# Optimization experiments

Hardware: AMD Instinct MI355X
Metric: run time of the kernel (lower is better)

## Reference

```python
import jax, jax.numpy as jnp
import numpy as np

N_QUBITS = 10
N_LAYERS = 4
BATCH = 2048


def setup_inputs() -> dict:
    key = jax.random.key(0)
    k1, k2 = jax.random.split(key)
    x = jax.random.normal(k1, (BATCH, N_QUBITS), dtype=jnp.float32)
    q_params = jax.random.normal(k2, (N_LAYERS * N_QUBITS * 3,), dtype=jnp.float32) * 0.01
    return {"x": x, "q_params": q_params}


def _apply_1q(state, U, wire):
    # state: (B, 2, 2, ..., 2); U: (2, 2) complex. Applies U on `wire`.
    s = jnp.moveaxis(state, wire + 1, -1)
    s = jnp.einsum('...j,ij->...i', s, U)
    return jnp.moveaxis(s, -1, wire + 1)


def _apply_cnot(state, ctrl, tgt):
    # flip target amplitude pair where control bit == 1
    s = jnp.moveaxis(state, (ctrl + 1, tgt + 1), (-2, -1))
    s = jnp.concatenate([s[..., 0:1, :], s[..., 1:2, ::-1]], axis=-2)
    return jnp.moveaxis(s, (-2, -1), (ctrl + 1, tgt + 1))


def _forward(x, q_params):
    B = x.shape[0]
    n, L = N_QUBITS, N_LAYERS
    # --- data-encoding layer: RY(x_i)|0> = [cos(x_i/2), sin(x_i/2)] per qubit ---
    half = 0.5 * x
    amps = jnp.stack([jnp.cos(half), jnp.sin(half)], axis=-1).astype(jnp.complex64)  # (B, n, 2)
    state = amps[:, 0, :]
    for i in range(1, n):  # build product state via successive kron (loop over n_qubits only)
        state = (state[:, :, None] * amps[:, i, None, :]).reshape(B, -1)
    state = state.reshape((B,) + (2,) * n)
    # --- variational gate matrices: per (layer, qubit) fused U = RZ @ RY @ RX ---
    w = q_params.reshape(L, n, 3)
    c, s = jnp.cos(0.5 * w), jnp.sin(0.5 * w)
    cx = c[..., 0].astype(jnp.complex64); sx = s[..., 0].astype(jnp.complex64)
    cy = c[..., 1].astype(jnp.complex64); sy = s[..., 1].astype(jnp.complex64)
    ez = jnp.exp(-0.5j * w[..., 2].astype(jnp.complex64))
    zeros = jnp.zeros_like(ez)
    Urx = jnp.stack([jnp.stack([cx, -1j * sx], -1), jnp.stack([-1j * sx, cx], -1)], -2)  # (L,n,2,2)
    Ury = jnp.stack([jnp.stack([cy, -sy], -1), jnp.stack([sy, cy], -1)], -2)
    Urz = jnp.stack([jnp.stack([ez, zeros], -1), jnp.stack([zeros, jnp.conj(ez)], -1)], -2)
    U = jnp.einsum('lnab,lnbc,lncd->lnad', Urz, Ury, Urx)  # apply order: RX then RY then RZ
    # --- circuit layers ---
    for l in range(L):
        for i in range(n):
            state = _apply_1q(state, U[l, i], i)
        for i in range(n - 1):
            state = _apply_cnot(state, i, i + 1)
    # --- <Z_i> expectation values ---
    p = jnp.abs(state) ** 2  # (B, 2, ..., 2) real probabilities
    evs = []
    for i in range(n):
        axes = tuple(a for a in range(1, n + 1) if a != i + 1)
        pi = jnp.sum(p, axis=axes)  # (B, 2)
        evs.append(pi[:, 0] - pi[:, 1])
    return jnp.stack(evs, axis=-1)  # (B, n_qubits)


def reference(x, q_params):
    return _forward(x, q_params)
```

## Files before the change

### kernel.cpp

```cpp
#include <hip/hip_runtime.h>
#include <math.h>

#define NQ 10
#define NL 4
#define NGATES (NL * NQ)
#define NTHREADS 256
#define BPW 2
#define WAVES 4

typedef float f32x2 __attribute__((ext_vector_type(2)));

#if __has_builtin(__builtin_amdgcn_permlane32_swap)
#define HAVE_PLSWAP 1
#else
#define HAVE_PLSWAP 0
#endif


template<int XM>
__device__ __forceinline__ float exch1(float v, bool selP) {
    if constexpr (XM == 0) return v;
    int x = __float_as_int(v);
    constexpr int low = XM & 31;
    if constexpr (low == 1)      x = __builtin_amdgcn_mov_dpp(x, 0xB1, 0xF, 0xF, true);
    else if constexpr (low == 2) x = __builtin_amdgcn_mov_dpp(x, 0x4E, 0xF, 0xF, true);
    else if constexpr (low == 3) x = __builtin_amdgcn_mov_dpp(x, 0x1B, 0xF, 0xF, true);
    else if constexpr (low != 0) x = __builtin_amdgcn_ds_swizzle(x, (low << 10) | 0x1F);
    if constexpr ((XM & 32) != 0) {
#if HAVE_PLSWAP
        auto r = __builtin_amdgcn_permlane32_swap((unsigned)x, (unsigned)x, false, false);
        x = selP ? (int)r[0] : (int)r[1];
#else
        x = __float_as_int(__shfl_xor(__int_as_float(x), 32, 64));
#endif
    }
    return __int_as_float(x);
}

template<int XM>
__device__ __forceinline__ f32x2 exch2(f32x2 v, bool selP) {
    f32x2 r;
    r.x = exch1<XM>(v.x, selP);
    r.y = exch1<XM>(v.y, selP);
    return r;
}

__device__ __forceinline__ f32x2 cfma4(f32x2 A, f32x2 st, f32x2 B, f32x2 pst) {
    f32x2 t;
    asm("v_pk_mul_f32 %0, %1, %2 op_sel:[0,0] op_sel_hi:[0,1]\n\t"
        "v_pk_fma_f32 %0, %1, %2, %0 op_sel:[1,1,0] op_sel_hi:[1,0,1] neg_lo:[0,1,0]\n\t"
        "v_pk_fma_f32 %0, %3, %4, %0 op_sel:[0,0,0] op_sel_hi:[0,1,1]\n\t"
        "v_pk_fma_f32 %0, %3, %4, %0 op_sel:[1,1,0] op_sel_hi:[1,0,1] neg_lo:[0,1,0]"
        : "=&v"(t)
        : "v"(A), "v"(st), "v"(B), "v"(pst));
    return t;
}

template<int XM, int XR, int SL, int SR>
__device__ __forceinline__ void gate2(f32x2 (&sa)[16], f32x2 (&sb)[16],
                                      const f32x2 (&g4)[4], int lane, bool selP) {
    bool hl = (SL != 0) && ((__popc(lane & SL) & 1) != 0);
    f32x2 A0, B0, A1, B1;
    A0.x = hl ? g4[3].x : g4[0].x;  A0.y = hl ? g4[3].y : g4[0].y;
    B0.x = hl ? g4[2].x : g4[1].x;  B0.y = hl ? g4[2].y : g4[1].y;
    A1.x = hl ? g4[0].x : g4[3].x;  A1.y = hl ? g4[0].y : g4[3].y;
    B1.x = hl ? g4[1].x : g4[2].x;  B1.y = hl ? g4[1].y : g4[2].y;
    f32x2 pa[16], pb[16];
    #pragma unroll
    for (int r = 0; r < 16; ++r) {
        pa[r] = exch2<XM>(sa[r ^ XR], selP);
        pb[r] = exch2<XM>(sb[r ^ XR], selP);
    }
    #pragma unroll
    for (int r = 0; r < 16; ++r) {
        const bool p1 = (__builtin_popcount(r & SR) & 1) != 0;
        f32x2 Ar = p1 ? A1 : A0;
        f32x2 Br = p1 ? B1 : B0;
        sa[r] = cfma4(Ar, sa[r], Br, pa[r]);
        sb[r] = cfma4(Ar, sb[r], Br, pb[r]);
    }
}

__device__ __forceinline__ float wht6(float v, int lane, bool selP) {
    float t;
    t = exch1<1>(v, selP);   v = (lane & 1)  ? (t - v) : (v + t);
    t = exch1<2>(v, selP);   v = (lane & 2)  ? (t - v) : (v + t);
    t = exch1<4>(v, selP);   v = (lane & 4)  ? (t - v) : (v + t);
    t = exch1<8>(v, selP);   v = (lane & 8)  ? (t - v) : (v + t);
    t = exch1<16>(v, selP);  v = (lane & 16) ? (t - v) : (v + t);
    t = exch1<32>(v, selP);  v = (lane & 32) ? (t - v) : (v + t);
    return v;
}

__device__ __forceinline__ void init_state(const float* __restrict__ x, int b,
                                           int lane, f32x2 (&st)[16]) {
    float c[NQ], s[NQ];
    #pragma unroll
    for (int q = 0; q < NQ; ++q) {
        float h = 0.5f * x[b * NQ + q];
        c[q] = __cosf(h);  s[q] = __sinf(h);
    }
    float lf = ((lane & 16) ? s[0] : c[0]) * ((lane & 8) ? s[1] : c[1]) *
               ((lane &  4) ? s[2] : c[2]) * ((lane & 32) ? s[7] : c[7]) *
               ((lane &  2) ? s[8] : c[8]) * ((lane &  1) ? s[9] : c[9]);
    #pragma unroll
    for (int r = 0; r < 16; ++r) {
        st[r].x = lf * ((r & 8) ? s[3] : c[3]) * ((r & 4) ? s[4] : c[4]) *
                       ((r & 2) ? s[5] : c[5]) * ((r & 1) ? s[6] : c[6]);
        st[r].y = 0.0f;
    }
}

__device__ __forceinline__ void epilogue(const f32x2 (&st)[16], int lane,
                                         bool selP, float* __restrict__ o) {
    float p[16];
    #pragma unroll
    for (int r = 0; r < 16; ++r) p[r] = st[r].x * st[r].x + st[r].y * st[r].y;
    float a[8], f8 = 0.0f;
    #pragma unroll
    for (int r = 0; r < 8; ++r) { a[r] = p[r] + p[r + 8]; f8 += p[r] - p[r + 8]; }
    float c4[4], f4 = 0.0f;
    #pragma unroll
    for (int r = 0; r < 4; ++r) { c4[r] = a[r] + a[r + 4]; f4 += a[r] - a[r + 4]; }
    float e2[2], f2 = 0.0f;
    #pragma unroll
    for (int r = 0; r < 2; ++r) { e2[r] = c4[r] + c4[r + 2]; f2 += c4[r] - c4[r + 2]; }
    float P  = e2[0] + e2[1];
    float f1 = e2[0] - e2[1];

    float wP = wht6(P,  lane, selP);
    float w8 = wht6(f8, lane, selP);
    float w4 = wht6(f4, lane, selP);
    float w2 = wht6(f2, lane, selP);
    float w1 = wht6(f1, lane, selP);

    if (lane == 16) { o[0] = wP; o[4] = w4; }
    if (lane ==  8) { o[1] = wP; o[5] = w2; }
    if (lane ==  4) { o[2] = wP; o[6] = w1; }
    if (lane ==  0) { o[3] = w8; }
    if (lane == 32) { o[7] = w8; }
    if (lane == 18) { o[8] = w4; }
    if (lane ==  9) { o[9] = w2; }
}

__global__ __launch_bounds__(NTHREADS, 1) void qlayer_kernel(
    const float* __restrict__ x,
    const float* __restrict__ qp,
    float* __restrict__ out,
    int B)
{
    __shared__ f32x2 su[NGATES][4];

    const int t = threadIdx.x;
    if (t < NGATES) {
        float w0 = qp[t * 3 + 0], w1 = qp[t * 3 + 1], w2 = qp[t * 3 + 2];
        float cx = __cosf(0.5f * w0), sx = __sinf(0.5f * w0);
        float cy = __cosf(0.5f * w1), sy = __sinf(0.5f * w1);
        float er = __cosf(0.5f * w2), ei = -__sinf(0.5f * w2);
        float m00r =  cy * cx, m00i =  sy * sx;
        float m01r = -sy * cx, m01i = -cy * sx;
        float m10r =  sy * cx, m10i = -cy * sx;
        float m11r =  cy * cx, m11i = -sy * sx;
        f32x2 v;
        v.x = er * m00r - ei * m00i;  v.y = er * m00i + ei * m00r;  su[t][0] = v;
        v.x = er * m01r - ei * m01i;  v.y = er * m01i + ei * m01r;  su[t][1] = v;
        v.x = er * m10r + ei * m10i;  v.y = er * m10i - ei * m10r;  su[t][2] = v;
        v.x = er * m11r + ei * m11i;  v.y = er * m11i - ei * m11r;  su[t][3] = v;
    }
    __syncthreads();

    const int lane = t & 63;
    const int wave = t >> 6;
    const int b0 = (blockIdx.x * WAVES + wave) * BPW;
    if (b0 >= B) return;

    bool selP = false;
#if HAVE_PLSWAP
    {
        auto pr = __builtin_amdgcn_permlane32_swap((unsigned)lane, (unsigned)lane, false, false);
        selP = ((int)pr[0] == (lane ^ 32));
    }
#endif

    f32x2 sa[16], sb[16];
    init_state(x, b0, lane, sa);
    init_state(x, (b0 + 1 < B) ? b0 + 1 : b0, lane, sb);

#define PREFETCH(L)                                                   \
    f32x2 cf[NQ][4];                                                  \
    _Pragma("unroll")                                                 \
    for (int q = 0; q < NQ; ++q) {                                    \
        cf[q][0] = su[(L)*NQ + q][0];  cf[q][1] = su[(L)*NQ + q][1];  \
        cf[q][2] = su[(L)*NQ + q][2];  cf[q][3] = su[(L)*NQ + q][3];  \
    }
#define GATE(Q, XM, XR, SLm, SRm) \
    gate2<XM, XR, SLm, SRm>(sa, sb, cf[Q], lane, selP);

    {
        PREFETCH(0)
        GATE(0, 16,0, 16,0)  GATE(1, 8,0, 8,0)    GATE(2, 4,0, 4,0)
        GATE(3, 0,8, 0,8)    GATE(4, 0,4, 0,4)    GATE(5, 0,2, 0,2)
        GATE(6, 0,1, 0,1)    GATE(7, 32,0, 32,0)  GATE(8, 2,0, 2,0)
        GATE(9, 1,0, 1,0)
    }
    {
        PREFETCH(1)
        GATE(0, 24,0, 16,0)  GATE(1, 12,0, 24,0)  GATE(2, 4,8, 28,0)
        GATE(3, 0,12, 28,8)  GATE(4, 0,6, 28,12)  GATE(5, 0,3, 28,14)
        GATE(6, 32,1, 28,15) GATE(7, 34,0, 60,15) GATE(8, 3,0, 62,15)
        GATE(9, 1,0, 63,15)
    }
    {
        PREFETCH(2)
        GATE(0, 20,0, 16,0)  GATE(1, 8,8, 8,0)    GATE(2, 4,4, 20,0)
        GATE(3, 0,10, 8,8)   GATE(4, 0,5, 20,4)   GATE(5, 32,2, 8,10)
        GATE(6, 2,1, 20,5)   GATE(7, 33,0, 40,10) GATE(8, 2,0, 22,5)
        GATE(9, 1,0, 41,10)
    }
    {
        PREFETCH(3)
        GATE(0, 28,8, 16,0)  GATE(1, 12,12, 24,0) GATE(2, 4,14, 12,0)
        GATE(3, 0,15, 4,8)   GATE(4, 32,7, 16,12) GATE(5, 34,3, 24,6)
        GATE(6, 35,1, 12,3)  GATE(7, 35,0, 36,9)  GATE(8, 3,0, 50,12)
        GATE(9, 1,0, 27,6)
    }
#undef GATE
#undef PREFETCH

    epilogue(sa, lane, selP, out + b0 * NQ);
    if (b0 + 1 < B) epilogue(sb, lane, selP, out + (b0 + 1) * NQ);
}

extern "C" void kernel_launch(void* const* d_in, const int* in_sizes, int n_in,
                              void* d_out, int out_size, void* d_ws, size_t ws_size,
                              hipStream_t stream) {
    const float* x  = (const float*)d_in[0];
    const float* qp = (const float*)d_in[1];
    float* out = (float*)d_out;
    const int B = in_sizes[0] / NQ;
    const int bpb = WAVES * BPW;
    const int blocks = (B + bpb - 1) / bpb;
    qlayer_kernel<<<blocks, NTHREADS, 0, stream>>>(x, qp, out, B);
}
```

Before: 80.74 us.

## Remap qubits to lanes for DPP/permlane exchanges, one sample per wave

Qubit-to-lane bits are reassigned so that most cross-lane exchanges use DPP row operations (row_mirror, row_half_mirror, quad perms) or permlane16/32 swaps instead of ds_swizzle. Each wave now simulates one batch sample instead of two, which doubles the grid, halves register state, and allows two blocks per CU via launch bounds. The aim is lower cross-lane exchange latency and more waves in flight to hide it, at the cost of less ILP per wave and a recomputed gate schedule and output lane mapping that must stay correct.

```diff
diff --git a/kernel.cpp b/kernel.cpp
--- a/kernel.cpp
+++ b/kernel.cpp
@@ -5,31 +5,52 @@
 #define NL 4
 #define NGATES (NL * NQ)
 #define NTHREADS 256
-#define BPW 2
-#define WAVES 4
+#define WPB 4
 
 typedef float f32x2 __attribute__((ext_vector_type(2)));
 
 #if __has_builtin(__builtin_amdgcn_permlane32_swap)
-#define HAVE_PLSWAP 1
-#else
-#define HAVE_PLSWAP 0
+#define HAVE_PL32 1
+#else
+#define HAVE_PL32 0
+#endif
+#if __has_builtin(__builtin_amdgcn_permlane16_swap)
+#define HAVE_PL16 1
+#else
+#define HAVE_PL16 0
 #endif
 
 
 template<int XM>
-__device__ __forceinline__ float exch1(float v, bool selP) {
+__device__ __forceinline__ float exch1(float v, bool sp32, bool sp16) {
     if constexpr (XM == 0) return v;
     int x = __float_as_int(v);
     constexpr int low = XM & 31;
-    if constexpr (low == 1)      x = __builtin_amdgcn_mov_dpp(x, 0xB1, 0xF, 0xF, true);
-    else if constexpr (low == 2) x = __builtin_amdgcn_mov_dpp(x, 0x4E, 0xF, 0xF, true);
-    else if constexpr (low == 3) x = __builtin_amdgcn_mov_dpp(x, 0x1B, 0xF, 0xF, true);
-    else if constexpr (low != 0) x = __builtin_amdgcn_ds_swizzle(x, (low << 10) | 0x1F);
+    if constexpr (low == 1)       x = __builtin_amdgcn_mov_dpp(x, 0xB1, 0xF, 0xF, true);
+    else if constexpr (low == 2)  x = __builtin_amdgcn_mov_dpp(x, 0x4E, 0xF, 0xF, true);
+    else if constexpr (low == 3)  x = __builtin_amdgcn_mov_dpp(x, 0x1B, 0xF, 0xF, true);
+    else if constexpr (low == 7)  x = __builtin_amdgcn_mov_dpp(x, 0x141, 0xF, 0xF, true);
+    else if constexpr (low == 8)  x = __builtin_amdgcn_mov_dpp(x, 0x128, 0xF, 0xF, true);
+    else if constexpr (low == 9)  { x = __builtin_amdgcn_mov_dpp(x, 0x128, 0xF, 0xF, true);
+                                    x = __builtin_amdgcn_mov_dpp(x, 0xB1, 0xF, 0xF, true); }
+    else if constexpr (low == 10) { x = __builtin_amdgcn_mov_dpp(x, 0x128, 0xF, 0xF, true);
+                                    x = __builtin_amdgcn_mov_dpp(x, 0x4E, 0xF, 0xF, true); }
+    else if constexpr (low == 11) { x = __builtin_amdgcn_mov_dpp(x, 0x128, 0xF, 0xF, true);
+                                    x = __builtin_amdgcn_mov_dpp(x, 0x1B, 0xF, 0xF, true); }
+    else if constexpr (low == 15) x = __builtin_amdgcn_mov_dpp(x, 0x140, 0xF, 0xF, true);
+    else if constexpr (low == 16) {
+#if HAVE_PL16
+        auto r = __builtin_amdgcn_permlane16_swap((unsigned)x, (unsigned)x, false, false);
+        x = sp16 ? (int)r[0] : (int)r[1];
+#else
+        x = __builtin_amdgcn_ds_swizzle(x, (16 << 10) | 0x1F);
+#endif
+    }
+    else if constexpr (low != 0)  x = __builtin_amdgcn_ds_swizzle(x, (low << 10) | 0x1F);
     if constexpr ((XM & 32) != 0) {
-#if HAVE_PLSWAP
+#if HAVE_PL32
         auto r = __builtin_amdgcn_permlane32_swap((unsigned)x, (unsigned)x, false, false);
-        x = selP ? (int)r[0] : (int)r[1];
+        x = sp32 ? (int)r[0] : (int)r[1];
 #else
         x = __float_as_int(__shfl_xor(__int_as_float(x), 32, 64));
 #endif
@@ -38,10 +59,10 @@
 }
 
 template<int XM>
-__device__ __forceinline__ f32x2 exch2(f32x2 v, bool selP) {
+__device__ __forceinline__ f32x2 exch2(f32x2 v, bool sp32, bool sp16) {
     f32x2 r;
-    r.x = exch1<XM>(v.x, selP);
-    r.y = exch1<XM>(v.y, selP);
+    r.x = exch1<XM>(v.x, sp32, sp16);
+    r.y = exch1<XM>(v.y, sp32, sp16);
     return r;
 }
 
@@ -57,93 +78,38 @@
 }
 
 template<int XM, int XR, int SL, int SR>
-__device__ __forceinline__ void gate2(f32x2 (&sa)[16], f32x2 (&sb)[16],
-                                      const f32x2 (&g4)[4], int lane, bool selP) {
+__device__ __forceinline__ void gate(f32x2 (&st)[16], const f32x2 (&g4)[4],
+                                     int lane, bool sp32, bool sp16) {
     bool hl = (SL != 0) && ((__popc(lane & SL) & 1) != 0);
     f32x2 A0, B0, A1, B1;
     A0.x = hl ? g4[3].x : g4[0].x;  A0.y = hl ? g4[3].y : g4[0].y;
     B0.x = hl ? g4[2].x : g4[1].x;  B0.y = hl ? g4[2].y : g4[1].y;
     A1.x = hl ? g4[0].x : g4[3].x;  A1.y = hl ? g4[0].y : g4[3].y;
     B1.x = hl ? g4[1].x : g4[2].x;  B1.y = hl ? g4[1].y : g4[2].y;
-    f32x2 pa[16], pb[16];
-    #pragma unroll
-    for (int r = 0; r < 16; ++r) {
-        pa[r] = exch2<XM>(sa[r ^ XR], selP);
-        pb[r] = exch2<XM>(sb[r ^ XR], selP);
-    }
+    f32x2 pst[16];
+    #pragma unroll
+    for (int r = 0; r < 16; ++r) pst[r] = exch2<XM>(st[r ^ XR], sp32, sp16);
     #pragma unroll
     for (int r = 0; r < 16; ++r) {
         const bool p1 = (__builtin_popcount(r & SR) & 1) != 0;
         f32x2 Ar = p1 ? A1 : A0;
         f32x2 Br = p1 ? B1 : B0;
-        sa[r] = cfma4(Ar, sa[r], Br, pa[r]);
-        sb[r] = cfma4(Ar, sb[r], Br, pb[r]);
-    }
-}
-
-__device__ __forceinline__ float wht6(float v, int lane, bool selP) {
+        st[r] = cfma4(Ar, st[r], Br, pst[r]);
+    }
+}
+
+__device__ __forceinline__ float wht6(float v, int lane, bool sp32, bool sp16) {
     float t;
-    t = exch1<1>(v, selP);   v = (lane & 1)  ? (t - v) : (v + t);
-    t = exch1<2>(v, selP);   v = (lane & 2)  ? (t - v) : (v + t);
-    t = exch1<4>(v, selP);   v = (lane & 4)  ? (t - v) : (v + t);
-    t = exch1<8>(v, selP);   v = (lane & 8)  ? (t - v) : (v + t);
-    t = exch1<16>(v, selP);  v = (lane & 16) ? (t - v) : (v + t);
-    t = exch1<32>(v, selP);  v = (lane & 32) ? (t - v) : (v + t);
+    t = exch1<1>(v, sp32, sp16);   v = (lane & 1)  ? (t - v) : (v + t);
+    t = exch1<2>(v, sp32, sp16);   v = (lane & 2)  ? (t - v) : (v + t);
+    t = exch1<4>(v, sp32, sp16);   v = (lane & 4)  ? (t - v) : (v + t);
+    t = exch1<8>(v, sp32, sp16);   v = (lane & 8)  ? (t - v) : (v + t);
+    t = exch1<16>(v, sp32, sp16);  v = (lane & 16) ? (t - v) : (v + t);
+    t = exch1<32>(v, sp32, sp16);  v = (lane & 32) ? (t - v) : (v + t);
     return v;
 }
 
-__device__ __forceinline__ void init_state(const float* __restrict__ x, int b,
-                                           int lane, f32x2 (&st)[16]) {
-    float c[NQ], s[NQ];
-    #pragma unroll
-    for (int q = 0; q < NQ; ++q) {
-        float h = 0.5f * x[b * NQ + q];
-        c[q] = __cosf(h);  s[q] = __sinf(h);
-    }
-    float lf = ((lane & 16) ? s[0] : c[0]) * ((lane & 8) ? s[1] : c[1]) *
-               ((lane &  4) ? s[2] : c[2]) * ((lane & 32) ? s[7] : c[7]) *
-               ((lane &  2) ? s[8] : c[8]) * ((lane &  1) ? s[9] : c[9]);
-    #pragma unroll
-    for (int r = 0; r < 16; ++r) {
-        st[r].x = lf * ((r & 8) ? s[3] : c[3]) * ((r & 4) ? s[4] : c[4]) *
-                       ((r & 2) ? s[5] : c[5]) * ((r & 1) ? s[6] : c[6]);
-        st[r].y = 0.0f;
-    }
-}
-
-__device__ __forceinline__ void epilogue(const f32x2 (&st)[16], int lane,
-                                         bool selP, float* __restrict__ o) {
-    float p[16];
-    #pragma unroll
-    for (int r = 0; r < 16; ++r) p[r] = st[r].x * st[r].x + st[r].y * st[r].y;
-    float a[8], f8 = 0.0f;
-    #pragma unroll
-    for (int r = 0; r < 8; ++r) { a[r] = p[r] + p[r + 8]; f8 += p[r] - p[r + 8]; }
-    float c4[4], f4 = 0.0f;
-    #pragma unroll
-    for (int r = 0; r < 4; ++r) { c4[r] = a[r] + a[r + 4]; f4 += a[r] - a[r + 4]; }
-    float e2[2], f2 = 0.0f;
-    #pragma unroll
-    for (int r = 0; r < 2; ++r) { e2[r] = c4[r] + c4[r + 2]; f2 += c4[r] - c4[r + 2]; }
-    float P  = e2[0] + e2[1];
-    float f1 = e2[0] - e2[1];
-
-    float wP = wht6(P,  lane, selP);
-    float w8 = wht6(f8, lane, selP);
-    float w4 = wht6(f4, lane, selP);
-    float w2 = wht6(f2, lane, selP);
-    float w1 = wht6(f1, lane, selP);
-
-    if (lane == 16) { o[0] = wP; o[4] = w4; }
-    if (lane ==  8) { o[1] = wP; o[5] = w2; }
-    if (lane ==  4) { o[2] = wP; o[6] = w1; }
-    if (lane ==  0) { o[3] = w8; }
-    if (lane == 32) { o[7] = w8; }
-    if (lane == 18) { o[8] = w4; }
-    if (lane ==  9) { o[9] = w2; }
-}
-
-__global__ __launch_bounds__(NTHREADS, 1) void qlayer_kernel(
+__global__ __launch_bounds__(NTHREADS, 2) void qlayer_kernel(
     const float* __restrict__ x,
     const float* __restrict__ qp,
     float* __restrict__ out,
@@ -170,21 +136,40 @@
     __syncthreads();
 
     const int lane = t & 63;
-    const int wave = t >> 6;
-    const int b0 = (blockIdx.x * WAVES + wave) * BPW;
-    if (b0 >= B) return;
-
-    bool selP = false;
-#if HAVE_PLSWAP
+    const int b = blockIdx.x * WPB + (t >> 6);
+    if (b >= B) return;
+
+    bool sp32 = false, sp16 = false;
+#if HAVE_PL32
     {
         auto pr = __builtin_amdgcn_permlane32_swap((unsigned)lane, (unsigned)lane, false, false);
-        selP = ((int)pr[0] == (lane ^ 32));
-    }
-#endif
-
-    f32x2 sa[16], sb[16];
-    init_state(x, b0, lane, sa);
-    init_state(x, (b0 + 1 < B) ? b0 + 1 : b0, lane, sb);
+        sp32 = ((int)pr[0] == (lane ^ 32));
+    }
+#endif
+#if HAVE_PL16
+    {
+        auto pr = __builtin_amdgcn_permlane16_swap((unsigned)lane, (unsigned)lane, false, false);
+        sp16 = ((int)pr[0] == (lane ^ 16));
+    }
+#endif
+
+    float c[NQ], s[NQ];
+    #pragma unroll
+    for (int q = 0; q < NQ; ++q) {
+        float h = 0.5f * x[b * NQ + q];
+        c[q] = __cosf(h);  s[q] = __sinf(h);
+    }
+
+    float lf = ((lane &  4) ? s[0] : c[0]) * ((lane & 32) ? s[1] : c[1]) *
+               ((lane & 16) ? s[2] : c[2]) * ((lane &  8) ? s[7] : c[7]) *
+               ((lane &  2) ? s[8] : c[8]) * ((lane &  1) ? s[9] : c[9]);
+    f32x2 st[16];
+    #pragma unroll
+    for (int r = 0; r < 16; ++r) {
+        st[r].x = lf * ((r & 8) ? s[3] : c[3]) * ((r & 4) ? s[4] : c[4]) *
+                       ((r & 2) ? s[5] : c[5]) * ((r & 1) ? s[6] : c[6]);
+        st[r].y = 0.0f;
+    }
 
 #define PREFETCH(L)                                                   \
     f32x2 cf[NQ][4];                                                  \
@@ -194,41 +179,68 @@
         cf[q][2] = su[(L)*NQ + q][2];  cf[q][3] = su[(L)*NQ + q][3];  \
     }
 #define GATE(Q, XM, XR, SLm, SRm) \
-    gate2<XM, XR, SLm, SRm>(sa, sb, cf[Q], lane, selP);
+    gate<XM, XR, SLm, SRm>(st, cf[Q], lane, sp32, sp16);
 
     {
         PREFETCH(0)
-        GATE(0, 16,0, 16,0)  GATE(1, 8,0, 8,0)    GATE(2, 4,0, 4,0)
-        GATE(3, 0,8, 0,8)    GATE(4, 0,4, 0,4)    GATE(5, 0,2, 0,2)
-        GATE(6, 0,1, 0,1)    GATE(7, 32,0, 32,0)  GATE(8, 2,0, 2,0)
+        GATE(0, 4,0, 4,0)     GATE(1, 32,0, 32,0)  GATE(2, 16,0, 16,0)
+        GATE(3, 0,8, 0,8)     GATE(4, 0,4, 0,4)    GATE(5, 0,2, 0,2)
+        GATE(6, 0,1, 0,1)     GATE(7, 8,0, 8,0)    GATE(8, 2,0, 2,0)
         GATE(9, 1,0, 1,0)
     }
     {
         PREFETCH(1)
-        GATE(0, 24,0, 16,0)  GATE(1, 12,0, 24,0)  GATE(2, 4,8, 28,0)
-        GATE(3, 0,12, 28,8)  GATE(4, 0,6, 28,12)  GATE(5, 0,3, 28,14)
-        GATE(6, 32,1, 28,15) GATE(7, 34,0, 60,15) GATE(8, 3,0, 62,15)
+        GATE(0, 36,0, 4,0)    GATE(1, 48,0, 36,0)  GATE(2, 16,8, 52,0)
+        GATE(3, 0,12, 52,8)   GATE(4, 0,6, 52,12)  GATE(5, 0,3, 52,14)
+        GATE(6, 8,1, 52,15)   GATE(7, 10,0, 60,15) GATE(8, 3,0, 62,15)
         GATE(9, 1,0, 63,15)
     }
     {
         PREFETCH(2)
-        GATE(0, 20,0, 16,0)  GATE(1, 8,8, 8,0)    GATE(2, 4,4, 20,0)
-        GATE(3, 0,10, 8,8)   GATE(4, 0,5, 20,4)   GATE(5, 32,2, 8,10)
-        GATE(6, 2,1, 20,5)   GATE(7, 33,0, 40,10) GATE(8, 2,0, 22,5)
+        GATE(0, 20,0, 4,0)    GATE(1, 32,8, 32,0)  GATE(2, 16,4, 20,0)
+        GATE(3, 0,10, 32,8)   GATE(4, 0,5, 20,4)   GATE(5, 8,2, 32,10)
+        GATE(6, 2,1, 20,5)    GATE(7, 9,0, 40,10)  GATE(8, 2,0, 22,5)
         GATE(9, 1,0, 41,10)
     }
     {
         PREFETCH(3)
-        GATE(0, 28,8, 16,0)  GATE(1, 12,12, 24,0) GATE(2, 4,14, 12,0)
-        GATE(3, 0,15, 4,8)   GATE(4, 32,7, 16,12) GATE(5, 34,3, 24,6)
-        GATE(6, 35,1, 12,3)  GATE(7, 35,0, 36,9)  GATE(8, 3,0, 50,12)
-        GATE(9, 1,0, 27,6)
+        GATE(0, 52,8, 4,0)    GATE(1, 48,12, 36,0) GATE(2, 16,14, 48,0)
+        GATE(3, 0,15, 16,8)   GATE(4, 8,7, 4,12)   GATE(5, 10,3, 36,6)
+        GATE(6, 11,1, 48,3)   GATE(7, 11,0, 24,9)  GATE(8, 3,0, 14,12)
+        GATE(9, 1,0, 39,6)
     }
 #undef GATE
 #undef PREFETCH
 
-    epilogue(sa, lane, selP, out + b0 * NQ);
-    if (b0 + 1 < B) epilogue(sb, lane, selP, out + (b0 + 1) * NQ);
+    float p[16];
+    #pragma unroll
+    for (int r = 0; r < 16; ++r) p[r] = st[r].x * st[r].x + st[r].y * st[r].y;
+    float a[8], f8 = 0.0f;
+    #pragma unroll
+    for (int r = 0; r < 8; ++r) { a[r] = p[r] + p[r + 8]; f8 += p[r] - p[r + 8]; }
+    float c4[4], f4 = 0.0f;
+    #pragma unroll
+    for (int r = 0; r < 4; ++r) { c4[r] = a[r] + a[r + 4]; f4 += a[r] - a[r + 4]; }
+    float e2[2], f2 = 0.0f;
+    #pragma unroll
+    for (int r = 0; r < 2; ++r) { e2[r] = c4[r] + c4[r + 2]; f2 += c4[r] - c4[r + 2]; }
+    float P  = e2[0] + e2[1];
+    float f1 = e2[0] - e2[1];
+
+    float wP = wht6(P,  lane, sp32, sp16);
+    float w8 = wht6(f8, lane, sp32, sp16);
+    float w4 = wht6(f4, lane, sp32, sp16);
+    float w2 = wht6(f2, lane, sp32, sp16);
+    float w1 = wht6(f1, lane, sp32, sp16);
+
+    float* o = out + b * NQ;
+    if (lane ==  4) { o[0] = wP; o[4] = w4; }
+    if (lane == 32) { o[1] = wP; o[5] = w2; }
+    if (lane == 16) { o[2] = wP; o[6] = w1; }
+    if (lane ==  0) { o[3] = w8; }
+    if (lane ==  8) { o[7] = w8; }
+    if (lane ==  6) { o[8] = w4; }
+    if (lane == 33) { o[9] = w2; }
 }
 
 extern "C" void kernel_launch(void* const* d_in, const int* in_sizes, int n_in,
@@ -238,7 +250,6 @@
     const float* qp = (const float*)d_in[1];
     float* out = (float*)d_out;
     const int B = in_sizes[0] / NQ;
-    const int bpb = WAVES * BPW;
-    const int blocks = (B + bpb - 1) / bpb;
+    const int blocks = (B + WPB - 1) / WPB;
     qlayer_kernel<<<blocks, NTHREADS, 0, stream>>>(x, qp, out, B);
 }
```

New measurement: 77.23 us. 4.4% less time.
